# Kernel optimization log

Measured on AMD Instinct MI355X. Metric: run time of the kernel, lower is better.

## Reference

```python
import jax, jax.numpy as jnp
import numpy as np

B, S, HOPS, DIM, NREL = 1024, 32, 2, 64, 237
NENT, NEDGE = 14541, 272115
SIGMA = 0.1
CFMW = 64


def setup_inputs() -> dict:
    key = jax.random.key(0)
    ks = jax.random.split(key, 20)

    def g(k, shape):
        return (jax.random.normal(k, shape, dtype=jnp.float32) / np.float32(np.sqrt(shape[0])))

    inp = {
        "entity_pairs": jax.random.randint(ks[0], (B, 2), 0, NENT),
        "train_edges": jax.random.randint(ks[1], (B,), 0, NEDGE),
        "labels": jax.random.randint(ks[2], (B,), 0, NREL),
        "entity2edges": jax.random.randint(ks[3], (NENT + 1, S), 0, NEDGE + 1),
        "edge2entities": jax.random.randint(ks[4], (NEDGE + 1, 1), 0, NENT + 1),
        "edge2relation": jax.random.randint(ks[5], (NEDGE + 1,), 0, NREL + 1),
        "t": jax.random.uniform(ks[6], (B,), dtype=jnp.float32),
        "eps": jax.random.normal(ks[7], (B, NREL), dtype=jnp.float32),
        "rel_feat": g(ks[8], (NREL, DIM)),
        "W_agg0": g(ks[9], (DIM, DIM)), "b_agg0": jnp.zeros((DIM,), jnp.float32),
        "W_agg1": g(ks[10], (DIM, NREL)), "b_agg1": jnp.zeros((NREL,), jnp.float32),
        "W_out": g(ks[11], (2 * NREL, NREL)), "b_out": jnp.zeros((NREL,), jnp.float32),
        "mW1": g(ks[12], (NREL + 1, CFMW)), "mb1": jnp.zeros((CFMW,), jnp.float32),
        "mW2": g(ks[13], (CFMW, CFMW)), "mb2": jnp.zeros((CFMW,), jnp.float32),
        "mW3": g(ks[14], (CFMW, CFMW)), "mb3": jnp.zeros((CFMW,), jnp.float32),
        "mW4": g(ks[15], (CFMW, NREL)), "mb4": jnp.zeros((NREL,), jnp.float32),
    }
    return inp


def _side(ent, labels, train_edges, entity2edges, edge2entities, edge2relation, relf, aggs):
    # multi-hop neighbor edge gather + masks (exclude the training edge itself)
    edges_list = [labels]  # hop-0 "edges" are the relation labels
    masks = []
    for i in range(HOPS):
        if i == 0:
            ne = ent.reshape(B, 1)  # (B, 1) source entities
        else:
            ne = edge2entities[edges_list[-1].reshape(-1)].reshape(B, -1)
        nedges = entity2edges[ne.reshape(-1)].reshape(B, -1)  # (B, S**(i+1))
        edges_list.append(nedges)
        masks.append((nedges != train_edges[:, None]).astype(relf.dtype))
    # edge -> relation -> feature
    ev = [relf[edges_list[0]]]  # (B, DIM)
    for edges in edges_list[1:]:
        ev.append(relf[edge2relation[edges]])  # (B, S**h, DIM)
    # iterative mean aggregation (PathCon-style, one entity per edge)
    for i in range(HOPS):
        W, b, act, self_inc = aggs[i]
        d = W.shape[0]
        nxt = []
        for hop in range(HOPS - i):
            neigh = ev[hop + 1].reshape(B, -1, 1, S, d)
            m = masks[hop].reshape(B, -1, 1, S, 1)
            out = jnp.mean(jnp.mean(neigh * m, axis=-2), axis=-2)  # (B, S**hop, d)
            if self_inc:
                out = out + ev[hop].reshape(B, -1, d)
            nxt.append(act(out @ W + b))
        ev = nxt
    return ev[0].reshape(B, NREL)


def reference(entity_pairs, train_edges, labels, entity2edges, edge2entities,
              edge2relation, t, eps, rel_feat, W_agg0, b_agg0, W_agg1, b_agg1,
              W_out, b_out, mW1, mb1, mW2, mb2, mW3, mb3, mW4, mb4):
    relf = jnp.concatenate([rel_feat, jnp.zeros((1, DIM), rel_feat.dtype)], axis=0)
    aggs = [
        (W_agg0, b_agg0, jax.nn.relu, True),    # intermediate hop: relu, self-included
        (W_agg1, b_agg1, lambda x: x, False),   # last hop: identity, no self
    ]
    x0 = _side(entity_pairs[:, 0], labels, train_edges, entity2edges,
               edge2entities, edge2relation, relf, aggs)
    x1 = _side(entity_pairs[:, 1], labels, train_edges, entity2edges,
               edge2entities, edge2relation, relf, aggs)
    output = jnp.concatenate([x0, x1], axis=-1) @ W_out + b_out  # (B, NREL)
    # CFM: xt = (1-t) x0 + t x1 + sigma*eps ; ut = x1 - x0
    tb = t[:, None]
    xt = (1.0 - tb) * x0 + tb * x1 + SIGMA * eps
    h = jnp.concatenate([xt, tb], axis=-1)
    h = jax.nn.selu(h @ mW1 + mb1)
    h = jax.nn.selu(h @ mW2 + mb2)
    h = jax.nn.selu(h @ mW3 + mb3)
    vt = h @ mW4 + mb4
    scores = output * vt
    return scores
```

## Files before the change

### kernel.cpp

```cpp
#include <hip/hip_runtime.h>
#include <math.h>

#define BB 1024
#define S 32
#define DIM 64
#define NREL 237
#define NENT 14541
#define SIGMA 0.1f

#define OFS_WR    0
#define N_WR      (238*64)
#define OFS_WC0   15232
#define N_WC      (64*237)
#define OFS_WC1   (OFS_WC0 + N_WC)
#define OFS_BC    (OFS_WC1 + N_WC)
#define OFS_A     45872
#define OFS_WM    976560
#define OFS_PE    980656

#define LDS_BYTES 18688

__device__ __forceinline__ float selu_f(float x) {
    const float alpha = 1.6732632423543772f;
    const float scale = 1.0507009873554805f;
    return scale * (x > 0.f ? x : alpha * expm1f(x));
}

__global__ __launch_bounds__(512) void pre_kernel(
    const float* __restrict__ rel_feat, const float* __restrict__ W0,
    const float* __restrict__ W1, const float* __restrict__ mW1,
    const float* __restrict__ b1, const float* __restrict__ mb1,
    const float* __restrict__ eps,
    float* __restrict__ ws) {
    __shared__ float sm[2160];
    int blk = blockIdx.x;
    const int tid = threadIdx.x;

    if (blk < 30) {
        int idx = blk * 512 + tid;
        if (idx < 238 * 64) {
            int r = idx >> 6, o = idx & 63;
            float acc = 0.f;
            if (r < NREL) {
#pragma unroll 8
                for (int d = 0; d < 64; ++d)
                    acc += rel_feat[r * 64 + d] * W0[d * 64 + o];
            }
            ws[OFS_WR + idx] = acc;
        }
        return;
    }
    blk -= 30;
    if (blk < 8) {
        int o0 = blk * 8;
        const float* src = W1 + o0 * 237;
        for (int i = tid; i < 8 * 237; i += 512) sm[i] = src[i];
        __syncthreads();
        int w = tid >> 6, cl = tid & 63;
        const float* row = sm + w * 237;
        float a0 = 0.f, a1 = 0.f, a2 = 0.f, a3 = 0.f;
#pragma unroll
        for (int k = 0; k < 236; k += 4) {
            a0 += row[k]     * mW1[k * 64 + cl];
            a1 += row[k + 1] * mW1[(k + 1) * 64 + cl];
            a2 += row[k + 2] * mW1[(k + 2) * 64 + cl];
            a3 += row[k + 3] * mW1[(k + 3) * 64 + cl];
        }
        a0 += row[236] * mW1[236 * 64 + cl];
        ws[OFS_WM + (o0 + w) * 64 + cl] = (a0 + a1) + (a2 + a3);
        return;
    }
    blk -= 8;
    {
        int b0 = blk * 8;
        const float* esrc = eps + b0 * 237;
        for (int i = tid; i < 8 * 237; i += 512) sm[i] = esrc[i];
        for (int i = tid; i < 237; i += 512) sm[1920 + i] = b1[i];
        __syncthreads();
        int w = tid >> 6, cl = tid & 63;
        const float* ew = sm + w * 237;
        const float* bb = sm + 1920;
        float a0 = mb1[cl], a1 = 0.f, a2 = 0.f, a3 = 0.f;
#pragma unroll
        for (int k = 0; k < 236; k += 4) {
            a0 += (SIGMA * ew[k]     + bb[k])     * mW1[k * 64 + cl];
            a1 += (SIGMA * ew[k + 1] + bb[k + 1]) * mW1[(k + 1) * 64 + cl];
            a2 += (SIGMA * ew[k + 2] + bb[k + 2]) * mW1[(k + 2) * 64 + cl];
            a3 += (SIGMA * ew[k + 3] + bb[k + 3]) * mW1[(k + 3) * 64 + cl];
        }
        a0 += (SIGMA * ew[236] + bb[236]) * mW1[236 * 64 + cl];
        ws[OFS_PE + (b0 + w) * 64 + cl] = (a0 + a1) + (a2 + a3);
    }
}

__global__ __launch_bounds__(512) void mid_kernel(
    const int* __restrict__ e2e_tab, const int* __restrict__ e2r,
    const float* __restrict__ W1, const float* __restrict__ b1,
    const float* __restrict__ W_out, const float* __restrict__ b_out,
    float* __restrict__ ws) {
    __shared__ int   s_r[1024];
    __shared__ float red[512];
    int blk = blockIdx.x;
    const int tid = threadIdx.x;

    if (blk < 455) {
        const int grp = tid >> 4, c = tid & 15;
        const int ent = blk * 32 + grp;
        const bool ok = ent < (NENT + 1);
        if (ok) {
            int ea = e2e_tab[ent * S + c];
            int eb = e2e_tab[ent * S + 16 + c];
            s_r[grp * 32 + c] = e2r[ea];
            s_r[grp * 32 + 16 + c] = e2r[eb];
        }
        __syncthreads();
        if (ok) {
            const float4* Wr4 = (const float4*)(ws + OFS_WR);
            const int* rr = &s_r[grp * 32];
            float4 acc = make_float4(0.f, 0.f, 0.f, 0.f);
#pragma unroll
            for (int s = 0; s < 32; ++s) {
                float4 v = Wr4[rr[s] * 16 + c];
                acc.x += v.x; acc.y += v.y; acc.z += v.z; acc.w += v.w;
            }
            ((float4*)(ws + OFS_A))[ent * 16 + c] = acc;
        }
        return;
    }
    blk -= 455;
    if (blk < 512) {
        int half = blk >> 8;
        int lb = blk & 255;
        int o = lb >> 2, ct = lb & 3;
        int cl = tid & 63, q = tid >> 6;
        int c = ct * 64 + cl;
        const float* Wsrc = W_out + half * 237 * 237;
        float acc = 0.f;
        if (c < NREL) {
            int k0 = q * 30, k1 = (q == 7) ? 237 : (k0 + 30);
#pragma unroll 4
            for (int k = k0; k < k1; ++k)
                acc += W1[o * 237 + k] * Wsrc[k * 237 + c];
        }
        red[tid] = acc;
        __syncthreads();
        if (q == 0 && c < NREL) {
            float s = 0.f;
#pragma unroll
            for (int qq = 0; qq < 8; ++qq) s += red[qq * 64 + cl];
            ws[(half ? OFS_WC1 : OFS_WC0) + o * 237 + c] = s;
        }
        return;
    }
    blk -= 512;
    {
        int cl = tid & 63, q = tid >> 6;
        int c = blk * 64 + cl;
        float acc = 0.f;
        if (c < NREL) {
            int k0 = q * 30, k1 = (q == 7) ? 237 : (k0 + 30);
#pragma unroll 4
            for (int k = k0; k < k1; ++k)
                acc += b1[k] * (W_out[k * 237 + c] + W_out[(237 + k) * 237 + c]);
        }
        red[tid] = acc;
        __syncthreads();
        if (q == 0 && c < NREL) {
            float s = b_out[c];
#pragma unroll
            for (int qq = 0; qq < 8; ++qq) s += red[qq * 64 + cl];
            ws[OFS_BC + c] = s;
        }
    }
}

__global__ __launch_bounds__(512, 8) void gf_kernel(
    const int* __restrict__ ep, const int* __restrict__ te_arr,
    const int* __restrict__ e2e_tab, const int* __restrict__ e2ent,
    const int* __restrict__ e2r, const float* __restrict__ b0,
    const float* __restrict__ t_arr,
    const float* __restrict__ mW1,
    const float* __restrict__ mW2, const float* __restrict__ mb2,
    const float* __restrict__ mW3, const float* __restrict__ mb3,
    const float* __restrict__ mW4, const float* __restrict__ mb4,
    const float* __restrict__ ws, float* __restrict__ out) {
    extern __shared__ float smem[];
    float* s_v1   = smem;
    int*   s_r1   = (int*)(smem + 4352);
    int*   s_ent2 = (int*)(smem + 4416);
    float* s_m1   = smem + 4480;
    float* s_ov   = smem + 4544;

    const int tid = threadIdx.x;
    const int b = blockIdx.x;
    const int grp = tid >> 4;
    const int c = tid & 15;
    const int te = te_arr[b];
    const int rte = e2r[te];
    const float4* Wr4 = (const float4*)(ws + OFS_WR);
    const float4* A4  = (const float4*)(ws + OFS_A);
    const float4 b0v  = ((const float4*)b0)[c];
    const float4 wrte = Wr4[rte * 16 + c];

    if (tid < 64) {
        int u = tid >> 5, s = tid & 31;
        int ent = ep[b * 2 + u];
        int e1 = e2e_tab[ent * S + s];
        s_r1[u * 32 + s] = e2r[e1];
        s_m1[u * 32 + s] = (e1 != te) ? 1.0f : 0.0f;
        s_ent2[u * 32 + s] = e2ent[e1];
    }
    __syncthreads();

    const float inv = 1.0f / 32.0f;
#pragma unroll
    for (int u = 0; u < 2; ++u) {
        const int j = grp;
        const int ent2 = s_ent2[u * 32 + j];
        int e2a = e2e_tab[ent2 * S + c];
        int e2b = e2e_tab[ent2 * S + 16 + c];
        int cnt = (e2a == te) + (e2b == te);
        cnt += __shfl_xor(cnt, 1);
        cnt += __shfl_xor(cnt, 2);
        cnt += __shfl_xor(cnt, 4);
        cnt += __shfl_xor(cnt, 8);
        float4 a4   = A4[ent2 * 16 + c];
        float4 self = Wr4[s_r1[u * 32 + j] * 16 + c];
        float fc = (float)cnt;
        float m = s_m1[u * 32 + j];
        float4 r;
        r.x = fmaxf(self.x + (a4.x - fc * wrte.x) * inv + b0v.x, 0.f) * m;
        r.y = fmaxf(self.y + (a4.y - fc * wrte.y) * inv + b0v.y, 0.f) * m;
        r.z = fmaxf(self.z + (a4.z - fc * wrte.z) * inv + b0v.z, 0.f) * m;
        r.w = fmaxf(self.w + (a4.w - fc * wrte.w) * inv + b0v.w, 0.f) * m;
        *((float4*)&s_v1[(u * 32 + j) * 68 + c * 4]) = r;
    }
    __syncthreads();
    if (tid < 128) {
        int u = tid >> 6, w = tid & 63;
        float sum = 0.f;
#pragma unroll 8
        for (int j = 0; j < 32; ++j) sum += s_v1[(u * 32 + j) * 68 + w];
        s_ov[u * 64 + w] = sum * inv;
    }
    __syncthreads();

    float* s_outp = smem;
    float* s_vp   = smem + 480;
    float* s_hA   = smem + 960;
    float* s_hB   = smem + 1024;
    float* s_omix = smem + 1088;
    const float tb = t_arr[b];
    const float* Wc0 = ws + OFS_WC0;
    const float* Wc1 = ws + OFS_WC1;
    const float* bc  = ws + OFS_BC;
    const float* Wm  = ws + OFS_WM;
    const float* pe  = ws + OFS_PE + b * 64;

    if (tid < 64)
        s_omix[tid] = (1.f - tb) * s_ov[tid] + tb * s_ov[64 + tid];
    {
        int half = tid >> 8, cc = tid & 255;
        if (cc < NREL) {
            const float* Wc  = half ? Wc1 : Wc0;
            const float* ovp = s_ov + half * 64;
            float a = 0.f;
#pragma unroll 4
            for (int d = 0; d < 64; ++d)
                a += ovp[d] * Wc[d * 237 + cc];
            s_outp[half * 240 + cc] = a;
        }
    }
    __syncthreads();

    if (tid < 64) {
        float a0 = pe[tid] + tb * mW1[237 * 64 + tid];
        float a1 = 0.f, a2 = 0.f, a3 = 0.f;
#pragma unroll
        for (int d = 0; d < 64; d += 4) {
            a0 += s_omix[d]     * Wm[d * 64 + tid];
            a1 += s_omix[d + 1] * Wm[(d + 1) * 64 + tid];
            a2 += s_omix[d + 2] * Wm[(d + 2) * 64 + tid];
            a3 += s_omix[d + 3] * Wm[(d + 3) * 64 + tid];
        }
        s_hA[tid] = selu_f((a0 + a1) + (a2 + a3));
    }
    __syncthreads();

    if (tid < 64) {
        float a0 = mb2[tid], a1 = 0.f, a2 = 0.f, a3 = 0.f;
#pragma unroll
        for (int d = 0; d < 64; d += 4) {
            a0 += s_hA[d]     * mW2[d * 64 + tid];
            a1 += s_hA[d + 1] * mW2[(d + 1) * 64 + tid];
            a2 += s_hA[d + 2] * mW2[(d + 2) * 64 + tid];
            a3 += s_hA[d + 3] * mW2[(d + 3) * 64 + tid];
        }
        s_hB[tid] = selu_f((a0 + a1) + (a2 + a3));
    }
    __syncthreads();

    if (tid < 64) {
        float a0 = mb3[tid], a1 = 0.f, a2 = 0.f, a3 = 0.f;
#pragma unroll
        for (int d = 0; d < 64; d += 4) {
            a0 += s_hB[d]     * mW3[d * 64 + tid];
            a1 += s_hB[d + 1] * mW3[(d + 1) * 64 + tid];
            a2 += s_hB[d + 2] * mW3[(d + 2) * 64 + tid];
            a3 += s_hB[d + 3] * mW3[(d + 3) * 64 + tid];
        }
        s_hA[tid] = selu_f((a0 + a1) + (a2 + a3));
    }
    __syncthreads();

    {
        int half = tid >> 8, cc = tid & 255;
        if (cc < NREL) {
            float a = 0.f;
#pragma unroll 4
            for (int w = half * 32; w < half * 32 + 32; ++w)
                a += s_hA[w] * mW4[w * 237 + cc];
            s_vp[half * 240 + cc] = a;
        }
    }
    __syncthreads();

    if (tid < NREL) {
        float outv = bc[tid] + s_outp[tid] + s_outp[240 + tid];
        out[b * 237 + tid] = outv * (mb4[tid] + s_vp[tid] + s_vp[240 + tid]);
    }
}

extern "C" void kernel_launch(void* const* d_in, const int* in_sizes, int n_in,
                              void* d_out, int out_size, void* d_ws, size_t ws_size,
                              hipStream_t stream) {
    const int* ep       = (const int*)d_in[0];
    const int* te       = (const int*)d_in[1];
    const int* e2e      = (const int*)d_in[3];
    const int* e2ent    = (const int*)d_in[4];
    const int* e2r      = (const int*)d_in[5];
    const float* t      = (const float*)d_in[6];
    const float* eps    = (const float*)d_in[7];
    const float* relf   = (const float*)d_in[8];
    const float* W0     = (const float*)d_in[9];
    const float* b0     = (const float*)d_in[10];
    const float* W1     = (const float*)d_in[11];
    const float* b1     = (const float*)d_in[12];
    const float* W_out  = (const float*)d_in[13];
    const float* b_out  = (const float*)d_in[14];
    const float* mW1    = (const float*)d_in[15];
    const float* mb1    = (const float*)d_in[16];
    const float* mW2    = (const float*)d_in[17];
    const float* mb2    = (const float*)d_in[18];
    const float* mW3    = (const float*)d_in[19];
    const float* mb3    = (const float*)d_in[20];
    const float* mW4    = (const float*)d_in[21];
    const float* mb4    = (const float*)d_in[22];
    float* ws  = (float*)d_ws;
    float* out = (float*)d_out;

    hipLaunchKernelGGL(pre_kernel, dim3(166), dim3(512), 0, stream,
                       relf, W0, W1, mW1, b1, mb1, eps, ws);
    hipLaunchKernelGGL(mid_kernel, dim3(971), dim3(512), 0, stream,
                       e2e, e2r, W1, b1, W_out, b_out, ws);
    hipLaunchKernelGGL(gf_kernel, dim3(BB), dim3(512), LDS_BYTES, stream,
                       ep, te, e2e, e2ent, e2r, b0,
                       t, mW1, mW2, mb2, mW3, mb3, mW4, mb4, ws, out);
}
```

Measured before the change: 137.6 us.

## Compress edge lookup tables to narrow ints and restructure W1·W_out precompute

Adds pre-kernel passes that pack edge2relation into uint8 and edge2entities into uint16 tables in the workspace, and the gather kernels read these instead of the int32 tables. The goal is a smaller random-gather footprint and better cache hit rates. The W1×W_out fused-weight computation now uses 16 blocks, each staging 8 rows of W1 in LDS and reusing every W_out load across 8 outputs, replacing 512 small blocks. The pre-kernel blocks are reordered and the packing costs an extra pass over about 1 MB of tables every call.

Measured after the change: 152.2 us. +10.6%, slower.

```diff
diff --git a/kernel.cpp b/kernel.cpp
--- a/kernel.cpp
+++ b/kernel.cpp
@@ -6,6 +6,7 @@
 #define DIM 64
 #define NREL 237
 #define NENT 14541
+#define NEDGE 272115
 #define SIGMA 0.1f
 
 #define OFS_WR    0
@@ -17,6 +18,9 @@
 #define OFS_A     45872
 #define OFS_WM    976560
 #define OFS_PE    980656
+#define OFS_E2R8  1046192
+#define OFS_E2E16 1114224
+#define NE2       272116
 
 #define LDS_BYTES 18688
 
@@ -31,11 +35,54 @@
     const float* __restrict__ W1, const float* __restrict__ mW1,
     const float* __restrict__ b1, const float* __restrict__ mb1,
     const float* __restrict__ eps,
+    const int* __restrict__ e2r, const int* __restrict__ e2ent,
     float* __restrict__ ws) {
     __shared__ float sm[2160];
     int blk = blockIdx.x;
     const int tid = threadIdx.x;
 
+    if (blk < 128) {
+        int b0 = blk * 8;
+        const float* esrc = eps + b0 * 237;
+        for (int i = tid; i < 8 * 237; i += 512) sm[i] = esrc[i];
+        for (int i = tid; i < 237; i += 512) sm[1920 + i] = b1[i];
+        __syncthreads();
+        int w = tid >> 6, cl = tid & 63;
+        const float* ew = sm + w * 237;
+        const float* bb = sm + 1920;
+        float a0 = mb1[cl], a1 = 0.f, a2 = 0.f, a3 = 0.f;
+#pragma unroll
+        for (int k = 0; k < 236; k += 4) {
+            a0 += (SIGMA * ew[k]     + bb[k])     * mW1[k * 64 + cl];
+            a1 += (SIGMA * ew[k + 1] + bb[k + 1]) * mW1[(k + 1) * 64 + cl];
+            a2 += (SIGMA * ew[k + 2] + bb[k + 2]) * mW1[(k + 2) * 64 + cl];
+            a3 += (SIGMA * ew[k + 3] + bb[k + 3]) * mW1[(k + 3) * 64 + cl];
+        }
+        a0 += (SIGMA * ew[236] + bb[236]) * mW1[236 * 64 + cl];
+        ws[OFS_PE + (b0 + w) * 64 + cl] = (a0 + a1) + (a2 + a3);
+        return;
+    }
+    blk -= 128;
+    if (blk < 8) {
+        int o0 = blk * 8;
+        const float* src = W1 + o0 * 237;
+        for (int i = tid; i < 8 * 237; i += 512) sm[i] = src[i];
+        __syncthreads();
+        int w = tid >> 6, cl = tid & 63;
+        const float* row = sm + w * 237;
+        float a0 = 0.f, a1 = 0.f, a2 = 0.f, a3 = 0.f;
+#pragma unroll
+        for (int k = 0; k < 236; k += 4) {
+            a0 += row[k]     * mW1[k * 64 + cl];
+            a1 += row[k + 1] * mW1[(k + 1) * 64 + cl];
+            a2 += row[k + 2] * mW1[(k + 2) * 64 + cl];
+            a3 += row[k + 3] * mW1[(k + 3) * 64 + cl];
+        }
+        a0 += row[236] * mW1[236 * 64 + cl];
+        ws[OFS_WM + (o0 + w) * 64 + cl] = (a0 + a1) + (a2 + a3);
+        return;
+    }
+    blk -= 8;
     if (blk < 30) {
         int idx = blk * 512 + tid;
         if (idx < 238 * 64) {
@@ -51,67 +98,49 @@
         return;
     }
     blk -= 30;
-    if (blk < 8) {
-        int o0 = blk * 8;
-        const float* src = W1 + o0 * 237;
-        for (int i = tid; i < 8 * 237; i += 512) sm[i] = src[i];
-        __syncthreads();
-        int w = tid >> 6, cl = tid & 63;
-        const float* row = sm + w * 237;
-        float a0 = 0.f, a1 = 0.f, a2 = 0.f, a3 = 0.f;
-#pragma unroll
-        for (int k = 0; k < 236; k += 4) {
-            a0 += row[k]     * mW1[k * 64 + cl];
-            a1 += row[k + 1] * mW1[(k + 1) * 64 + cl];
-            a2 += row[k + 2] * mW1[(k + 2) * 64 + cl];
-            a3 += row[k + 3] * mW1[(k + 3) * 64 + cl];
-        }
-        a0 += row[236] * mW1[236 * 64 + cl];
-        ws[OFS_WM + (o0 + w) * 64 + cl] = (a0 + a1) + (a2 + a3);
-        return;
-    }
-    blk -= 8;
+    if (blk < 133) {
+        int i = blk * 512 + tid;
+        if (i < 68029) {
+            int4 v = ((const int4*)e2r)[i];
+            uchar4 p;
+            p.x = (unsigned char)v.x; p.y = (unsigned char)v.y;
+            p.z = (unsigned char)v.z; p.w = (unsigned char)v.w;
+            ((uchar4*)(ws + OFS_E2R8))[i] = p;
+        }
+        return;
+    }
+    blk -= 133;
     {
-        int b0 = blk * 8;
-        const float* esrc = eps + b0 * 237;
-        for (int i = tid; i < 8 * 237; i += 512) sm[i] = esrc[i];
-        for (int i = tid; i < 237; i += 512) sm[1920 + i] = b1[i];
-        __syncthreads();
-        int w = tid >> 6, cl = tid & 63;
-        const float* ew = sm + w * 237;
-        const float* bb = sm + 1920;
-        float a0 = mb1[cl], a1 = 0.f, a2 = 0.f, a3 = 0.f;
-#pragma unroll
-        for (int k = 0; k < 236; k += 4) {
-            a0 += (SIGMA * ew[k]     + bb[k])     * mW1[k * 64 + cl];
-            a1 += (SIGMA * ew[k + 1] + bb[k + 1]) * mW1[(k + 1) * 64 + cl];
-            a2 += (SIGMA * ew[k + 2] + bb[k + 2]) * mW1[(k + 2) * 64 + cl];
-            a3 += (SIGMA * ew[k + 3] + bb[k + 3]) * mW1[(k + 3) * 64 + cl];
-        }
-        a0 += (SIGMA * ew[236] + bb[236]) * mW1[236 * 64 + cl];
-        ws[OFS_PE + (b0 + w) * 64 + cl] = (a0 + a1) + (a2 + a3);
+        int i = blk * 512 + tid;
+        if (i < 136058) {
+            int2 v = ((const int2*)e2ent)[i];
+            ushort2 p;
+            p.x = (unsigned short)v.x; p.y = (unsigned short)v.y;
+            ((ushort2*)(ws + OFS_E2E16))[i] = p;
+        }
     }
 }
 
 __global__ __launch_bounds__(512) void mid_kernel(
-    const int* __restrict__ e2e_tab, const int* __restrict__ e2r,
+    const int* __restrict__ e2e_tab,
     const float* __restrict__ W1, const float* __restrict__ b1,
     const float* __restrict__ W_out, const float* __restrict__ b_out,
     float* __restrict__ ws) {
-    __shared__ int   s_r[1024];
-    __shared__ float red[512];
+    __shared__ float smf[3952];
     int blk = blockIdx.x;
     const int tid = threadIdx.x;
 
     if (blk < 455) {
+        int* s_r = (int*)smf;
+        const unsigned char* e2r8 = (const unsigned char*)(ws + OFS_E2R8);
         const int grp = tid >> 4, c = tid & 15;
         const int ent = blk * 32 + grp;
         const bool ok = ent < (NENT + 1);
         if (ok) {
             int ea = e2e_tab[ent * S + c];
             int eb = e2e_tab[ent * S + 16 + c];
-            s_r[grp * 32 + c] = e2r[ea];
-            s_r[grp * 32 + 16 + c] = e2r[eb];
+            s_r[grp * 32 + c] = e2r8[ea];
+            s_r[grp * 32 + 16 + c] = e2r8[eb];
         }
         __syncthreads();
         if (ok) {
@@ -128,32 +157,43 @@
         return;
     }
     blk -= 455;
-    if (blk < 512) {
-        int half = blk >> 8;
-        int lb = blk & 255;
-        int o = lb >> 2, ct = lb & 3;
-        int cl = tid & 63, q = tid >> 6;
-        int c = ct * 64 + cl;
+    if (blk < 16) {
+        float* s_W1  = smf;
+        float* s_red = smf + 1896;
+        int half = blk >> 3;
+        int o0 = (blk & 7) * 8;
+        const float* src = W1 + o0 * 237;
+        for (int i = tid; i < 8 * 237; i += 512) s_W1[i] = src[i];
+        __syncthreads();
+        int q = tid >> 8, cc = tid & 255;
         const float* Wsrc = W_out + half * 237 * 237;
-        float acc = 0.f;
-        if (c < NREL) {
-            int k0 = q * 30, k1 = (q == 7) ? 237 : (k0 + 30);
-#pragma unroll 4
-            for (int k = k0; k < k1; ++k)
-                acc += W1[o * 237 + k] * Wsrc[k * 237 + c];
-        }
-        red[tid] = acc;
-        __syncthreads();
-        if (q == 0 && c < NREL) {
-            float s = 0.f;
-#pragma unroll
-            for (int qq = 0; qq < 8; ++qq) s += red[qq * 64 + cl];
-            ws[(half ? OFS_WC1 : OFS_WC0) + o * 237 + c] = s;
-        }
-        return;
-    }
-    blk -= 512;
+        float acc[8] = {0.f, 0.f, 0.f, 0.f, 0.f, 0.f, 0.f, 0.f};
+        if (cc < NREL) {
+            int k0 = q ? 119 : 0, k1 = q ? 237 : 119;
+#pragma unroll 2
+            for (int k = k0; k < k1; ++k) {
+                float w_ = Wsrc[k * 237 + cc];
+#pragma unroll
+                for (int o = 0; o < 8; ++o)
+                    acc[o] += s_W1[o * 237 + k] * w_;
+            }
+        }
+        if (q) {
+#pragma unroll
+            for (int o = 0; o < 8; ++o) s_red[o * 256 + cc] = acc[o];
+        }
+        __syncthreads();
+        if (!q && cc < NREL) {
+            float* dst = ws + (half ? OFS_WC1 : OFS_WC0);
+#pragma unroll
+            for (int o = 0; o < 8; ++o)
+                dst[(o0 + o) * 237 + cc] = acc[o] + s_red[o * 256 + cc];
+        }
+        return;
+    }
+    blk -= 16;
     {
+        float* red = smf;
         int cl = tid & 63, q = tid >> 6;
         int c = blk * 64 + cl;
         float acc = 0.f;
@@ -176,8 +216,7 @@
 
 __global__ __launch_bounds__(512, 8) void gf_kernel(
     const int* __restrict__ ep, const int* __restrict__ te_arr,
-    const int* __restrict__ e2e_tab, const int* __restrict__ e2ent,
-    const int* __restrict__ e2r, const float* __restrict__ b0,
+    const int* __restrict__ e2e_tab, const float* __restrict__ b0,
     const float* __restrict__ t_arr,
     const float* __restrict__ mW1,
     const float* __restrict__ mW2, const float* __restrict__ mb2,
@@ -195,8 +234,10 @@
     const int b = blockIdx.x;
     const int grp = tid >> 4;
     const int c = tid & 15;
+    const unsigned char*  e2r8    = (const unsigned char*)(ws + OFS_E2R8);
+    const unsigned short* e2ent16 = (const unsigned short*)(ws + OFS_E2E16);
     const int te = te_arr[b];
-    const int rte = e2r[te];
+    const int rte = e2r8[te];
     const float4* Wr4 = (const float4*)(ws + OFS_WR);
     const float4* A4  = (const float4*)(ws + OFS_A);
     const float4 b0v  = ((const float4*)b0)[c];
@@ -206,9 +247,9 @@
         int u = tid >> 5, s = tid & 31;
         int ent = ep[b * 2 + u];
         int e1 = e2e_tab[ent * S + s];
-        s_r1[u * 32 + s] = e2r[e1];
+        s_r1[u * 32 + s] = e2r8[e1];
         s_m1[u * 32 + s] = (e1 != te) ? 1.0f : 0.0f;
-        s_ent2[u * 32 + s] = e2ent[e1];
+        s_ent2[u * 32 + s] = e2ent16[e1];
     }
     __syncthreads();
 
@@ -359,11 +400,11 @@
     float* ws  = (float*)d_ws;
     float* out = (float*)d_out;
 
-    hipLaunchKernelGGL(pre_kernel, dim3(166), dim3(512), 0, stream,
-                       relf, W0, W1, mW1, b1, mb1, eps, ws);
-    hipLaunchKernelGGL(mid_kernel, dim3(971), dim3(512), 0, stream,
-                       e2e, e2r, W1, b1, W_out, b_out, ws);
+    hipLaunchKernelGGL(pre_kernel, dim3(565), dim3(512), 0, stream,
+                       relf, W0, W1, mW1, b1, mb1, eps, e2r, e2ent, ws);
+    hipLaunchKernelGGL(mid_kernel, dim3(475), dim3(512), 0, stream,
+                       e2e, W1, b1, W_out, b_out, ws);
     hipLaunchKernelGGL(gf_kernel, dim3(BB), dim3(512), LDS_BYTES, stream,
-                       ep, te, e2e, e2ent, e2r, b0,
+                       ep, te, e2e, b0,
                        t, mW1, mW2, mb2, mW3, mb3, mW4, mb4, ws, out);
 }
```

## Merge pre and mid kernels into one launch by reassociating entity aggregation

Applied to the files above, without the earlier changes.

The two setup kernels are fused into a single launch. To remove the dependency of the entity aggregation on the precomputed rel_feat@W0 table, each entity block now sums raw relation features (masking the padding relation) and then multiplies the sum by W0 in-kernel. This removes one kernel launch and the serialization between the two kernels, at the cost of a 64x64 matvec per entity, which is extra arithmetic. The WR table is still computed, presumably because gf_kernel reads it.

After: 145.6 us. +5.8%, slower.

```diff
diff --git a/kernel.cpp b/kernel.cpp
--- a/kernel.cpp
+++ b/kernel.cpp
@@ -26,84 +26,21 @@
     return scale * (x > 0.f ? x : alpha * expm1f(x));
 }
 
-__global__ __launch_bounds__(512) void pre_kernel(
+__global__ __launch_bounds__(512) void k1_kernel(
+    const int* __restrict__ e2e_tab, const int* __restrict__ e2r,
     const float* __restrict__ rel_feat, const float* __restrict__ W0,
-    const float* __restrict__ W1, const float* __restrict__ mW1,
-    const float* __restrict__ b1, const float* __restrict__ mb1,
+    const float* __restrict__ W1, const float* __restrict__ b1,
+    const float* __restrict__ W_out, const float* __restrict__ b_out,
+    const float* __restrict__ mW1, const float* __restrict__ mb1,
     const float* __restrict__ eps,
     float* __restrict__ ws) {
-    __shared__ float sm[2160];
+    __shared__ float smf[3392];
     int blk = blockIdx.x;
     const int tid = threadIdx.x;
 
-    if (blk < 30) {
-        int idx = blk * 512 + tid;
-        if (idx < 238 * 64) {
-            int r = idx >> 6, o = idx & 63;
-            float acc = 0.f;
-            if (r < NREL) {
-#pragma unroll 8
-                for (int d = 0; d < 64; ++d)
-                    acc += rel_feat[r * 64 + d] * W0[d * 64 + o];
-            }
-            ws[OFS_WR + idx] = acc;
-        }
-        return;
-    }
-    blk -= 30;
-    if (blk < 8) {
-        int o0 = blk * 8;
-        const float* src = W1 + o0 * 237;
-        for (int i = tid; i < 8 * 237; i += 512) sm[i] = src[i];
-        __syncthreads();
-        int w = tid >> 6, cl = tid & 63;
-        const float* row = sm + w * 237;
-        float a0 = 0.f, a1 = 0.f, a2 = 0.f, a3 = 0.f;
-#pragma unroll
-        for (int k = 0; k < 236; k += 4) {
-            a0 += row[k]     * mW1[k * 64 + cl];
-            a1 += row[k + 1] * mW1[(k + 1) * 64 + cl];
-            a2 += row[k + 2] * mW1[(k + 2) * 64 + cl];
-            a3 += row[k + 3] * mW1[(k + 3) * 64 + cl];
-        }
-        a0 += row[236] * mW1[236 * 64 + cl];
-        ws[OFS_WM + (o0 + w) * 64 + cl] = (a0 + a1) + (a2 + a3);
-        return;
-    }
-    blk -= 8;
-    {
-        int b0 = blk * 8;
-        const float* esrc = eps + b0 * 237;
-        for (int i = tid; i < 8 * 237; i += 512) sm[i] = esrc[i];
-        for (int i = tid; i < 237; i += 512) sm[1920 + i] = b1[i];
-        __syncthreads();
-        int w = tid >> 6, cl = tid & 63;
-        const float* ew = sm + w * 237;
-        const float* bb = sm + 1920;
-        float a0 = mb1[cl], a1 = 0.f, a2 = 0.f, a3 = 0.f;
-#pragma unroll
-        for (int k = 0; k < 236; k += 4) {
-            a0 += (SIGMA * ew[k]     + bb[k])     * mW1[k * 64 + cl];
-            a1 += (SIGMA * ew[k + 1] + bb[k + 1]) * mW1[(k + 1) * 64 + cl];
-            a2 += (SIGMA * ew[k + 2] + bb[k + 2]) * mW1[(k + 2) * 64 + cl];
-            a3 += (SIGMA * ew[k + 3] + bb[k + 3]) * mW1[(k + 3) * 64 + cl];
-        }
-        a0 += (SIGMA * ew[236] + bb[236]) * mW1[236 * 64 + cl];
-        ws[OFS_PE + (b0 + w) * 64 + cl] = (a0 + a1) + (a2 + a3);
-    }
-}
-
-__global__ __launch_bounds__(512) void mid_kernel(
-    const int* __restrict__ e2e_tab, const int* __restrict__ e2r,
-    const float* __restrict__ W1, const float* __restrict__ b1,
-    const float* __restrict__ W_out, const float* __restrict__ b_out,
-    float* __restrict__ ws) {
-    __shared__ int   s_r[1024];
-    __shared__ float red[512];
-    int blk = blockIdx.x;
-    const int tid = threadIdx.x;
-
     if (blk < 455) {
+        int*   s_r  = (int*)smf;
+        float* s_SR = smf + 1024;
         const int grp = tid >> 4, c = tid & 15;
         const int ent = blk * 32 + grp;
         const bool ok = ent < (NENT + 1);
@@ -115,20 +52,38 @@
         }
         __syncthreads();
         if (ok) {
-            const float4* Wr4 = (const float4*)(ws + OFS_WR);
+            const float4* R4 = (const float4*)rel_feat;
             const int* rr = &s_r[grp * 32];
             float4 acc = make_float4(0.f, 0.f, 0.f, 0.f);
 #pragma unroll
             for (int s = 0; s < 32; ++s) {
-                float4 v = Wr4[rr[s] * 16 + c];
-                acc.x += v.x; acc.y += v.y; acc.z += v.z; acc.w += v.w;
+                int r = rr[s];
+                float sc = (r < NREL) ? 1.0f : 0.0f;
+                float4 v = R4[(r < NREL ? r : 0) * 16 + c];
+                acc.x += sc * v.x; acc.y += sc * v.y;
+                acc.z += sc * v.z; acc.w += sc * v.w;
             }
-            ((float4*)(ws + OFS_A))[ent * 16 + c] = acc;
+            *((float4*)&s_SR[grp * 68 + c * 4]) = acc;
+        }
+        __syncthreads();
+        if (ok) {
+            const float4* W04 = (const float4*)W0;
+            const float* sr = &s_SR[grp * 68];
+            float4 a = make_float4(0.f, 0.f, 0.f, 0.f);
+#pragma unroll 8
+            for (int d = 0; d < 64; ++d) {
+                float sv = sr[d];
+                float4 w = W04[d * 16 + c];
+                a.x += sv * w.x; a.y += sv * w.y;
+                a.z += sv * w.z; a.w += sv * w.w;
+            }
+            ((float4*)(ws + OFS_A))[ent * 16 + c] = a;
         }
         return;
     }
     blk -= 455;
     if (blk < 512) {
+        float* red = smf;
         int half = blk >> 8;
         int lb = blk & 255;
         int o = lb >> 2, ct = lb & 3;
@@ -153,7 +108,8 @@
         return;
     }
     blk -= 512;
-    {
+    if (blk < 4) {
+        float* red = smf;
         int cl = tid & 63, q = tid >> 6;
         int c = blk * 64 + cl;
         float acc = 0.f;
@@ -171,6 +127,63 @@
             for (int qq = 0; qq < 8; ++qq) s += red[qq * 64 + cl];
             ws[OFS_BC + c] = s;
         }
+        return;
+    }
+    blk -= 4;
+    if (blk < 30) {
+        int idx = blk * 512 + tid;
+        if (idx < 238 * 64) {
+            int r = idx >> 6, o = idx & 63;
+            float acc = 0.f;
+            if (r < NREL) {
+#pragma unroll 8
+                for (int d = 0; d < 64; ++d)
+                    acc += rel_feat[r * 64 + d] * W0[d * 64 + o];
+            }
+            ws[OFS_WR + idx] = acc;
+        }
+        return;
+    }
+    blk -= 30;
+    if (blk < 8) {
+        int o0 = blk * 8;
+        const float* src = W1 + o0 * 237;
+        for (int i = tid; i < 8 * 237; i += 512) smf[i] = src[i];
+        __syncthreads();
+        int w = tid >> 6, cl = tid & 63;
+        const float* row = smf + w * 237;
+        float a0 = 0.f, a1 = 0.f, a2 = 0.f, a3 = 0.f;
+#pragma unroll
+        for (int k = 0; k < 236; k += 4) {
+            a0 += row[k]     * mW1[k * 64 + cl];
+            a1 += row[k + 1] * mW1[(k + 1) * 64 + cl];
+            a2 += row[k + 2] * mW1[(k + 2) * 64 + cl];
+            a3 += row[k + 3] * mW1[(k + 3) * 64 + cl];
+        }
+        a0 += row[236] * mW1[236 * 64 + cl];
+        ws[OFS_WM + (o0 + w) * 64 + cl] = (a0 + a1) + (a2 + a3);
+        return;
+    }
+    blk -= 8;
+    {
+        int b0 = blk * 8;
+        const float* esrc = eps + b0 * 237;
+        for (int i = tid; i < 8 * 237; i += 512) smf[i] = esrc[i];
+        for (int i = tid; i < 237; i += 512) smf[1920 + i] = b1[i];
+        __syncthreads();
+        int w = tid >> 6, cl = tid & 63;
+        const float* ew = smf + w * 237;
+        const float* bb = smf + 1920;
+        float a0 = mb1[cl], a1 = 0.f, a2 = 0.f, a3 = 0.f;
+#pragma unroll
+        for (int k = 0; k < 236; k += 4) {
+            a0 += (SIGMA * ew[k]     + bb[k])     * mW1[k * 64 + cl];
+            a1 += (SIGMA * ew[k + 1] + bb[k + 1]) * mW1[(k + 1) * 64 + cl];
+            a2 += (SIGMA * ew[k + 2] + bb[k + 2]) * mW1[(k + 2) * 64 + cl];
+            a3 += (SIGMA * ew[k + 3] + bb[k + 3]) * mW1[(k + 3) * 64 + cl];
+        }
+        a0 += (SIGMA * ew[236] + bb[236]) * mW1[236 * 64 + cl];
+        ws[OFS_PE + (b0 + w) * 64 + cl] = (a0 + a1) + (a2 + a3);
     }
 }
 
@@ -359,10 +372,9 @@
     float* ws  = (float*)d_ws;
     float* out = (float*)d_out;
 
-    hipLaunchKernelGGL(pre_kernel, dim3(166), dim3(512), 0, stream,
-                       relf, W0, W1, mW1, b1, mb1, eps, ws);
-    hipLaunchKernelGGL(mid_kernel, dim3(971), dim3(512), 0, stream,
-                       e2e, e2r, W1, b1, W_out, b_out, ws);
+    hipLaunchKernelGGL(k1_kernel, dim3(1137), dim3(512), 0, stream,
+                       e2e, e2r, relf, W0, W1, b1, W_out, b_out,
+                       mW1, mb1, eps, ws);
     hipLaunchKernelGGL(gf_kernel, dim3(BB), dim3(512), LDS_BYTES, stream,
                        ep, te, e2e, e2ent, e2r, b0,
                        t, mW1, mW2, mb2, mW3, mb3, mW4, mb4, ws, out);
```

## Split gather and MLP epilogue into separate kernels batching four rows per block

Applied to the files above, without the earlier changes.

The per-batch fused kernel is split in two. A gather kernel writes the two aggregated side vectors to workspace, and a new epilogue kernel handles four batch rows per block, so each weight load is reused across two rows and more threads stay busy in the small MLP layers. The pre-kernel block order is also changed so the larger eps projection blocks get scheduled first. The cost is one extra kernel launch and a round trip of the side vectors through global memory.

Measured after the change: 159.8 us. +16.2%, slower.

```diff
diff --git a/kernel.cpp b/kernel.cpp
--- a/kernel.cpp
+++ b/kernel.cpp
@@ -17,8 +17,9 @@
 #define OFS_A     45872
 #define OFS_WM    976560
 #define OFS_PE    980656
-
-#define LDS_BYTES 18688
+#define OFS_OV    1046192
+
+#define LDS_BYTES 18176
 
 __device__ __forceinline__ float selu_f(float x) {
     const float alpha = 1.6732632423543772f;
@@ -36,7 +37,49 @@
     int blk = blockIdx.x;
     const int tid = threadIdx.x;
 
-    if (blk < 30) {
+    if (blk < 128) {
+        int b0 = blk * 8;
+        const float* esrc = eps + b0 * 237;
+        for (int i = tid; i < 8 * 237; i += 512) sm[i] = esrc[i];
+        for (int i = tid; i < 237; i += 512) sm[1920 + i] = b1[i];
+        __syncthreads();
+        int w = tid >> 6, cl = tid & 63;
+        const float* ew = sm + w * 237;
+        const float* bb = sm + 1920;
+        float a0 = mb1[cl], a1 = 0.f, a2 = 0.f, a3 = 0.f;
+#pragma unroll
+        for (int k = 0; k < 236; k += 4) {
+            a0 += (SIGMA * ew[k]     + bb[k])     * mW1[k * 64 + cl];
+            a1 += (SIGMA * ew[k + 1] + bb[k + 1]) * mW1[(k + 1) * 64 + cl];
+            a2 += (SIGMA * ew[k + 2] + bb[k + 2]) * mW1[(k + 2) * 64 + cl];
+            a3 += (SIGMA * ew[k + 3] + bb[k + 3]) * mW1[(k + 3) * 64 + cl];
+        }
+        a0 += (SIGMA * ew[236] + bb[236]) * mW1[236 * 64 + cl];
+        ws[OFS_PE + (b0 + w) * 64 + cl] = (a0 + a1) + (a2 + a3);
+        return;
+    }
+    blk -= 128;
+    if (blk < 8) {
+        int o0 = blk * 8;
+        const float* src = W1 + o0 * 237;
+        for (int i = tid; i < 8 * 237; i += 512) sm[i] = src[i];
+        __syncthreads();
+        int w = tid >> 6, cl = tid & 63;
+        const float* row = sm + w * 237;
+        float a0 = 0.f, a1 = 0.f, a2 = 0.f, a3 = 0.f;
+#pragma unroll
+        for (int k = 0; k < 236; k += 4) {
+            a0 += row[k]     * mW1[k * 64 + cl];
+            a1 += row[k + 1] * mW1[(k + 1) * 64 + cl];
+            a2 += row[k + 2] * mW1[(k + 2) * 64 + cl];
+            a3 += row[k + 3] * mW1[(k + 3) * 64 + cl];
+        }
+        a0 += row[236] * mW1[236 * 64 + cl];
+        ws[OFS_WM + (o0 + w) * 64 + cl] = (a0 + a1) + (a2 + a3);
+        return;
+    }
+    blk -= 8;
+    {
         int idx = blk * 512 + tid;
         if (idx < 238 * 64) {
             int r = idx >> 6, o = idx & 63;
@@ -48,48 +91,6 @@
             }
             ws[OFS_WR + idx] = acc;
         }
-        return;
-    }
-    blk -= 30;
-    if (blk < 8) {
-        int o0 = blk * 8;
-        const float* src = W1 + o0 * 237;
-        for (int i = tid; i < 8 * 237; i += 512) sm[i] = src[i];
-        __syncthreads();
-        int w = tid >> 6, cl = tid & 63;
-        const float* row = sm + w * 237;
-        float a0 = 0.f, a1 = 0.f, a2 = 0.f, a3 = 0.f;
-#pragma unroll
-        for (int k = 0; k < 236; k += 4) {
-            a0 += row[k]     * mW1[k * 64 + cl];
-            a1 += row[k + 1] * mW1[(k + 1) * 64 + cl];
-            a2 += row[k + 2] * mW1[(k + 2) * 64 + cl];
-            a3 += row[k + 3] * mW1[(k + 3) * 64 + cl];
-        }
-        a0 += row[236] * mW1[236 * 64 + cl];
-        ws[OFS_WM + (o0 + w) * 64 + cl] = (a0 + a1) + (a2 + a3);
-        return;
-    }
-    blk -= 8;
-    {
-        int b0 = blk * 8;
-        const float* esrc = eps + b0 * 237;
-        for (int i = tid; i < 8 * 237; i += 512) sm[i] = esrc[i];
-        for (int i = tid; i < 237; i += 512) sm[1920 + i] = b1[i];
-        __syncthreads();
-        int w = tid >> 6, cl = tid & 63;
-        const float* ew = sm + w * 237;
-        const float* bb = sm + 1920;
-        float a0 = mb1[cl], a1 = 0.f, a2 = 0.f, a3 = 0.f;
-#pragma unroll
-        for (int k = 0; k < 236; k += 4) {
-            a0 += (SIGMA * ew[k]     + bb[k])     * mW1[k * 64 + cl];
-            a1 += (SIGMA * ew[k + 1] + bb[k + 1]) * mW1[(k + 1) * 64 + cl];
-            a2 += (SIGMA * ew[k + 2] + bb[k + 2]) * mW1[(k + 2) * 64 + cl];
-            a3 += (SIGMA * ew[k + 3] + bb[k + 3]) * mW1[(k + 3) * 64 + cl];
-        }
-        a0 += (SIGMA * ew[236] + bb[236]) * mW1[236 * 64 + cl];
-        ws[OFS_PE + (b0 + w) * 64 + cl] = (a0 + a1) + (a2 + a3);
     }
 }
 
@@ -174,22 +175,16 @@
     }
 }
 
-__global__ __launch_bounds__(512, 8) void gf_kernel(
+__global__ __launch_bounds__(512, 8) void gf_gather_kernel(
     const int* __restrict__ ep, const int* __restrict__ te_arr,
     const int* __restrict__ e2e_tab, const int* __restrict__ e2ent,
     const int* __restrict__ e2r, const float* __restrict__ b0,
-    const float* __restrict__ t_arr,
-    const float* __restrict__ mW1,
-    const float* __restrict__ mW2, const float* __restrict__ mb2,
-    const float* __restrict__ mW3, const float* __restrict__ mb3,
-    const float* __restrict__ mW4, const float* __restrict__ mb4,
-    const float* __restrict__ ws, float* __restrict__ out) {
+    const float* __restrict__ ws, float* __restrict__ ws_out) {
     extern __shared__ float smem[];
     float* s_v1   = smem;
     int*   s_r1   = (int*)(smem + 4352);
     int*   s_ent2 = (int*)(smem + 4416);
     float* s_m1   = smem + 4480;
-    float* s_ov   = smem + 4544;
 
     const int tid = threadIdx.x;
     const int b = blockIdx.x;
@@ -241,93 +236,106 @@
         float sum = 0.f;
 #pragma unroll 8
         for (int j = 0; j < 32; ++j) sum += s_v1[(u * 32 + j) * 68 + w];
-        s_ov[u * 64 + w] = sum * inv;
-    }
-    __syncthreads();
-
-    float* s_outp = smem;
-    float* s_vp   = smem + 480;
-    float* s_hA   = smem + 960;
-    float* s_hB   = smem + 1024;
-    float* s_omix = smem + 1088;
-    const float tb = t_arr[b];
-    const float* Wc0 = ws + OFS_WC0;
-    const float* Wc1 = ws + OFS_WC1;
-    const float* bc  = ws + OFS_BC;
-    const float* Wm  = ws + OFS_WM;
-    const float* pe  = ws + OFS_PE + b * 64;
-
-    if (tid < 64)
-        s_omix[tid] = (1.f - tb) * s_ov[tid] + tb * s_ov[64 + tid];
-    {
-        int half = tid >> 8, cc = tid & 255;
+        ws_out[OFS_OV + b * 128 + tid] = sum * inv;
+    }
+}
+
+__global__ __launch_bounds__(512, 4) void gf_epi_kernel(
+    const float* __restrict__ t_arr,
+    const float* __restrict__ mW1,
+    const float* __restrict__ mW2, const float* __restrict__ mb2,
+    const float* __restrict__ mW3, const float* __restrict__ mb3,
+    const float* __restrict__ mW4, const float* __restrict__ mb4,
+    const float* __restrict__ ws, float* __restrict__ out) {
+    __shared__ float s_ov[4][128];
+    __shared__ float s_outv[4][240];
+    __shared__ float s_hA[4][64];
+    __shared__ float s_hB[4][64];
+
+    const int tid = threadIdx.x;
+    const int b0 = blockIdx.x * 4;
+
+    {
+        int bl = tid >> 7, i = tid & 127;
+        s_ov[bl][i] = ws[OFS_OV + (b0 + bl) * 128 + i];
+    }
+    __syncthreads();
+
+    {
+        int cc = tid & 255, q = tid >> 8;
         if (cc < NREL) {
-            const float* Wc  = half ? Wc1 : Wc0;
-            const float* ovp = s_ov + half * 64;
-            float a = 0.f;
-#pragma unroll 4
-            for (int d = 0; d < 64; ++d)
-                a += ovp[d] * Wc[d * 237 + cc];
-            s_outp[half * 240 + cc] = a;
-        }
-    }
-    __syncthreads();
-
-    if (tid < 64) {
-        float a0 = pe[tid] + tb * mW1[237 * 64 + tid];
-        float a1 = 0.f, a2 = 0.f, a3 = 0.f;
-#pragma unroll
-        for (int d = 0; d < 64; d += 4) {
-            a0 += s_omix[d]     * Wm[d * 64 + tid];
-            a1 += s_omix[d + 1] * Wm[(d + 1) * 64 + tid];
-            a2 += s_omix[d + 2] * Wm[(d + 2) * 64 + tid];
-            a3 += s_omix[d + 3] * Wm[(d + 3) * 64 + tid];
-        }
-        s_hA[tid] = selu_f((a0 + a1) + (a2 + a3));
-    }
-    __syncthreads();
-
-    if (tid < 64) {
-        float a0 = mb2[tid], a1 = 0.f, a2 = 0.f, a3 = 0.f;
-#pragma unroll
-        for (int d = 0; d < 64; d += 4) {
-            a0 += s_hA[d]     * mW2[d * 64 + tid];
-            a1 += s_hA[d + 1] * mW2[(d + 1) * 64 + tid];
-            a2 += s_hA[d + 2] * mW2[(d + 2) * 64 + tid];
-            a3 += s_hA[d + 3] * mW2[(d + 3) * 64 + tid];
-        }
-        s_hB[tid] = selu_f((a0 + a1) + (a2 + a3));
-    }
-    __syncthreads();
-
-    if (tid < 64) {
-        float a0 = mb3[tid], a1 = 0.f, a2 = 0.f, a3 = 0.f;
-#pragma unroll
-        for (int d = 0; d < 64; d += 4) {
-            a0 += s_hB[d]     * mW3[d * 64 + tid];
-            a1 += s_hB[d + 1] * mW3[(d + 1) * 64 + tid];
-            a2 += s_hB[d + 2] * mW3[(d + 2) * 64 + tid];
-            a3 += s_hB[d + 3] * mW3[(d + 3) * 64 + tid];
-        }
-        s_hA[tid] = selu_f((a0 + a1) + (a2 + a3));
-    }
-    __syncthreads();
-
-    {
-        int half = tid >> 8, cc = tid & 255;
+            const float* Wc0 = ws + OFS_WC0;
+            const float* Wc1 = ws + OFS_WC1;
+            int ba = q * 2, bb_ = ba + 1;
+            float a0 = 0.f, a1 = 0.f;
+#pragma unroll 4
+            for (int d = 0; d < 64; ++d) {
+                float w0 = Wc0[d * 237 + cc];
+                a0 += s_ov[ba][d] * w0;
+                a1 += s_ov[bb_][d] * w0;
+            }
+#pragma unroll 4
+            for (int d = 0; d < 64; ++d) {
+                float w1 = Wc1[d * 237 + cc];
+                a0 += s_ov[ba][64 + d] * w1;
+                a1 += s_ov[bb_][64 + d] * w1;
+            }
+            float bcv = ws[OFS_BC + cc];
+            s_outv[ba][cc] = a0 + bcv;
+            s_outv[bb_][cc] = a1 + bcv;
+        }
+    }
+    __syncthreads();
+
+    if (tid < 256) {
+        int bl = tid >> 6, w = tid & 63;
+        float tb = t_arr[b0 + bl];
+        const float* Wm = ws + OFS_WM;
+        float acc = ws[OFS_PE + (b0 + bl) * 64 + w] + tb * mW1[237 * 64 + w];
+#pragma unroll 4
+        for (int d = 0; d < 64; ++d) {
+            float om = (1.f - tb) * s_ov[bl][d] + tb * s_ov[bl][64 + d];
+            acc += om * Wm[d * 64 + w];
+        }
+        s_hA[bl][w] = selu_f(acc);
+    }
+    __syncthreads();
+
+    if (tid < 256) {
+        int bl = tid >> 6, w = tid & 63;
+        float acc = mb2[w];
+#pragma unroll 4
+        for (int d = 0; d < 64; ++d)
+            acc += s_hA[bl][d] * mW2[d * 64 + w];
+        s_hB[bl][w] = selu_f(acc);
+    }
+    __syncthreads();
+
+    if (tid < 256) {
+        int bl = tid >> 6, w = tid & 63;
+        float acc = mb3[w];
+#pragma unroll 4
+        for (int d = 0; d < 64; ++d)
+            acc += s_hB[bl][d] * mW3[d * 64 + w];
+        s_hA[bl][w] = selu_f(acc);
+    }
+    __syncthreads();
+
+    {
+        int cc = tid & 255, q = tid >> 8;
         if (cc < NREL) {
-            float a = 0.f;
-#pragma unroll 4
-            for (int w = half * 32; w < half * 32 + 32; ++w)
-                a += s_hA[w] * mW4[w * 237 + cc];
-            s_vp[half * 240 + cc] = a;
-        }
-    }
-    __syncthreads();
-
-    if (tid < NREL) {
-        float outv = bc[tid] + s_outp[tid] + s_outp[240 + tid];
-        out[b * 237 + tid] = outv * (mb4[tid] + s_vp[tid] + s_vp[240 + tid]);
+            int ba = q * 2, bb_ = ba + 1;
+            float a0 = 0.f, a1 = 0.f;
+#pragma unroll 4
+            for (int w = 0; w < 64; ++w) {
+                float wv = mW4[w * 237 + cc];
+                a0 += s_hA[ba][w] * wv;
+                a1 += s_hA[bb_][w] * wv;
+            }
+            float m4 = mb4[cc];
+            out[(b0 + ba) * 237 + cc] = s_outv[ba][cc] * (m4 + a0);
+            out[(b0 + bb_) * 237 + cc] = s_outv[bb_][cc] * (m4 + a1);
+        }
     }
 }
 
@@ -363,7 +371,8 @@
                        relf, W0, W1, mW1, b1, mb1, eps, ws);
     hipLaunchKernelGGL(mid_kernel, dim3(971), dim3(512), 0, stream,
                        e2e, e2r, W1, b1, W_out, b_out, ws);
-    hipLaunchKernelGGL(gf_kernel, dim3(BB), dim3(512), LDS_BYTES, stream,
-                       ep, te, e2e, e2ent, e2r, b0,
+    hipLaunchKernelGGL(gf_gather_kernel, dim3(BB), dim3(512), LDS_BYTES, stream,
+                       ep, te, e2e, e2ent, e2r, b0, ws, ws);
+    hipLaunchKernelGGL(gf_epi_kernel, dim3(256), dim3(512), 0, stream,
                        t, mW1, mW2, mb2, mW3, mb3, mW4, mb4, ws, out);
 }
```
